# Optimization experiments

Hardware: AMD Instinct MI355X
Metric: run time of the kernel (lower is better)

Reference implementation:

```python
import jax, jax.numpy as jnp
import numpy as np
import math

NQ = 12          # num_qubits
DEPTH = 4        # circuit_depth
DIM = 2 ** NQ    # state_dim = 4096
B = 4096         # batch

# CNOT ladder: (i,i+1) plus wrap-around (n-1,0) when n>2 (as in _init_circuit_parameters)
CNOT_PAIRS = [(i, i + 1) for i in range(NQ - 1)] + ([(NQ - 1, 0)] if NQ > 2 else [])


def _rx(theta):
    c = jnp.cos(theta / 2).astype(jnp.complex64)
    s = jnp.sin(theta / 2).astype(jnp.complex64) * (-1j)
    return jnp.stack([jnp.stack([c, s]), jnp.stack([s, c])])


def _ry(phi):
    c = jnp.cos(phi / 2).astype(jnp.complex64)
    s = jnp.sin(phi / 2).astype(jnp.complex64)
    return jnp.stack([jnp.stack([c, -s]), jnp.stack([s, c])])


def _rz(lam):
    lamc = lam.astype(jnp.complex64)
    e0 = jnp.exp(-1j * lamc / 2)
    e1 = jnp.exp(1j * lamc / 2)
    z = jnp.zeros((), jnp.complex64)
    return jnp.stack([jnp.stack([e0, z]), jnp.stack([z, e1])])


def _apply_1q(state, gate, q):
    # state: [B] + [2]*NQ, qubit q lives on axis q+1 (kron order: qubit 0 most significant)
    ax = q + 1
    s = jnp.moveaxis(state, ax, -1)
    s = jnp.einsum('ab,...b->...a', gate, s)
    return jnp.moveaxis(s, -1, ax)


def _apply_cnot(state, control, target):
    # flip target bit on the control=1 half of the state vector
    ac, at = control + 1, target + 1
    s0 = jnp.take(state, jnp.array([0]), axis=ac)
    s1 = jnp.take(state, jnp.array([1]), axis=ac)
    s1 = jnp.flip(s1, axis=at)
    return jnp.concatenate([s0, s1], axis=ac)


def setup_inputs() -> dict:
    key = jax.random.key(0)
    k1, k2, k3, k4 = jax.random.split(key, 4)
    return {
        'input_data': jax.random.normal(k1, (B, DIM), dtype=jnp.float32),
        'angles_x': jax.random.normal(k2, (DEPTH, NQ), dtype=jnp.float32) * 0.5,
        'angles_y': jax.random.normal(k3, (DEPTH, NQ), dtype=jnp.float32) * 0.5,
        'angles_z': jax.random.normal(k4, (DEPTH, NQ), dtype=jnp.float32) * 0.5,
    }


def reference(input_data, angles_x, angles_y, angles_z):
    # --- amplitude encoding (faithful to quantum_weight_memory) ---
    w = jnp.abs(input_data[:, :DIM])                      # [B, D]
    D = w.shape[1]
    s = jnp.sum(w, axis=1, keepdims=True)
    wn = jnp.where(s > 1e-8, w / jnp.sqrt(jnp.maximum(s, 1e-8)),
                   jnp.full_like(w, 1.0 / math.sqrt(D)))
    state = jnp.zeros((w.shape[0], DIM), jnp.complex64).at[:, 0].set(1.0)
    state = state.at[:, :D].set(wn.astype(jnp.complex64))
    norm = jnp.sqrt(jnp.sum(jnp.abs(state) ** 2, axis=1, keepdims=True))
    state = jnp.where(norm > 1e-8, state / jnp.maximum(norm, 1e-8), state)

    # --- parametrized circuit, applied as local state-vector updates ---
    state = state.reshape((state.shape[0],) + (2,) * NQ)
    for layer in range(DEPTH):
        for q in range(NQ):
            state = _apply_1q(state, _rx(angles_x[layer, q]), q)
            state = _apply_1q(state, _ry(angles_y[layer, q]), q)
            state = _apply_1q(state, _rz(angles_z[layer, q]), q)
        for c, t in CNOT_PAIRS:
            state = _apply_cnot(state, c, t)
    state = state.reshape(-1, DIM)

    # --- measurement ---
    probs = jnp.abs(state) ** 2
    return jnp.sqrt(probs[:, :DIM])
```

## Files before the change

kernel.cpp:

```cpp
#include <hip/hip_runtime.h>
#include <math.h>

#define DIM 4096

typedef _Float16 v8h __attribute__((ext_vector_type(8)));
typedef _Float16 v4h __attribute__((ext_vector_type(4)));
typedef float v4f __attribute__((ext_vector_type(4)));
typedef unsigned int v2u __attribute__((ext_vector_type(2)));

__device__ __forceinline__ int adr(int row, int off) {
  return ((row << 6) | off) ^ ((((row >> 1) ^ (row >> 5)) & 3) << 4)
                            ^ (((row >> 4) & 1) << 6);
}


template <int PASS, bool FOLD>
__device__ __forceinline__ void do_pass(const char* __restrict__ src, char* __restrict__ dst,
                                        const v8h* __restrict__ Af, int mat, int t) {
  const int lane = t & 63, wv = t >> 6;
  const int m = lane & 15, q = lane >> 4;
  const int qb = q & 1, pm = q >> 1;
  const v8h b_re = Af[(mat * 2 + 0) * 64 + lane];
  const v8h b_im = Af[(mat * 2 + 1) * 64 + lane];
  const int gm = (m ^ (m >> 1)) & 15;
#pragma unroll
  for (int tt = 0; tt < 4; ++tt) {
    const int t4 = wv * 4 + tt;
    v8h a;
    if constexpr (PASS == 0 && FOLD) {
      const int t4g = t4 ^ (t4 >> 1);
      const bool qs = ((qb ^ tt) & 1) != 0;
      const int off = pm * 32 + (qs ? 16 : 0);
      const int r0 = ((t4g ^ ((m & 1) << 3)) << 4) | gm;
      const uint4 E = *(const uint4*)(src + adr(r0, off));
      const uint4 O = *(const uint4*)(src + adr(r0 ^ 8, off));
      const unsigned e0 = qs ? E.z : E.x, e1 = qs ? E.w : E.y;
      const unsigned e2 = qs ? E.y : E.w, e3 = qs ? E.x : E.z;
      const unsigned o0 = qs ? O.z : O.x, o1 = qs ? O.w : O.y;
      const unsigned o2 = qs ? O.y : O.w, o3 = qs ? O.x : O.z;
      uint4 av;
      av.x = __builtin_amdgcn_perm(o0, e0, 0x07060100u);
      av.y = __builtin_amdgcn_perm(o1, e1, 0x05040302u);
      av.z = __builtin_amdgcn_perm(o2, e2, 0x07060100u);
      av.w = __builtin_amdgcn_perm(o3, e3, 0x05040302u);
      a = __builtin_bit_cast(v8h, av);
    } else if constexpr (PASS == 0) {
      a = *(const v8h*)(src + adr(t4 * 16 + m, pm * 32 + qb * 16));
    } else {
      const uint4 r = *(const uint4*)(src + adr(t4 * 16 + m, (2 * qb + pm) * 16));
      const v2u s0 = __builtin_amdgcn_permlane32_swap(r.x, r.z, false, false);
      const v2u s1 = __builtin_amdgcn_permlane32_swap(r.y, r.w, false, false);
      uint4 av;
      av.x = s0.x; av.y = s1.x; av.z = s0.y; av.w = s1.y;
      a = __builtin_bit_cast(v8h, av);
    }
    const v4f cre = __builtin_amdgcn_mfma_f32_16x16x32_f16(a, b_re, (v4f){0.f, 0.f, 0.f, 0.f}, 0, 0, 0);
    const v4f cim = __builtin_amdgcn_mfma_f32_16x16x32_f16(a, b_im, (v4f){0.f, 0.f, 0.f, 0.f}, 0, 0, 0);
    const int wrow = m * 16 + t4;
    if constexpr (PASS < 2) {
      v8h w;
#pragma unroll
      for (int r2 = 0; r2 < 4; ++r2) {
        w[r2] = (_Float16)cre[r2];
        w[4 + r2] = (_Float16)cim[r2];
      }
      *(v8h*)(dst + adr(wrow, q * 16)) = w;
    } else {
      v4h wre, wim;
#pragma unroll
      for (int r2 = 0; r2 < 4; ++r2) {
        wre[r2] = (_Float16)cre[r2];
        wim[r2] = (_Float16)cim[r2];
      }
      *(v4h*)(dst + adr(wrow, q * 8)) = wre;
      *(v4h*)(dst + adr(wrow, 32 + q * 8)) = wim;
    }
  }
}

__global__ void make_gates2(const float* __restrict__ ax, const float* __restrict__ ay,
                            const float* __restrict__ az, _Float16* __restrict__ Aw) {
  __shared__ float g4[48][4];
  const int id = threadIdx.x;
  if (id < 48) {
    float th = 0.5f * ax[id], ph = 0.5f * ay[id], lm = 0.5f * az[id];
    float c = cosf(th), s = sinf(th);
    float cy = cosf(ph), sy = sinf(ph);
    float cl = cosf(lm), sl = sinf(lm);
    float m00r = cy * c, m00i = sy * s;
    float m01r = -sy * c, m01i = -cy * s;
    g4[id][0] = cl * m00r + sl * m00i;
    g4[id][1] = cl * m00i - sl * m00r;
    g4[id][2] = cl * m01r + sl * m01i;
    g4[id][3] = cl * m01i - sl * m01r;
  }
  __syncthreads();
  const int mat = id >> 6, lane = id & 63;
  const int m = lane & 15, q = lane >> 4;
  const int layer = mat / 3, pass = mat % 3, qbase = pass * 4;
#pragma unroll
  for (int j = 0; j < 8; ++j) {
    const int k = q * 8 + j, kk = k & 15;
    float cr = 1.f, ci = 0.f;
#pragma unroll
    for (int bp = 3; bp >= 0; --bp) {
      const int qq = qbase + (3 - bp);
      const int ib = (m >> bp) & 1, kb = (kk >> bp) & 1;
      const float* gg = g4[layer * 12 + qq];
      float er, ei;
      if (ib == 0 && kb == 0) { er = gg[0]; ei = gg[1]; }
      else if (ib == 0 && kb == 1) { er = gg[2]; ei = gg[3]; }
      else if (ib == 1 && kb == 0) { er = -gg[2]; ei = gg[3]; }
      else { er = gg[0]; ei = -gg[1]; }
      const float nr = cr * er - ci * ei, ni = cr * ei + ci * er;
      cr = nr; ci = ni;
    }
    const float reval = (k < 16) ? cr : -ci;
    const float imval = (k < 16) ? ci : cr;
    Aw[((mat * 2 + 0) * 64 + lane) * 8 + j] = (_Float16)reval;
    Aw[((mat * 2 + 1) * 64 + lane) * 8 + j] = (_Float16)imval;
  }
}

__global__ __launch_bounds__(256, 4) void qsim4(const float* __restrict__ x,
                                                const v8h* __restrict__ Af,
                                                float* __restrict__ out) {
  __shared__ __align__(16) char buf[2][16384];
  const int t = threadIdx.x;
  const int b = blockIdx.x;
  const float* xb = x + (size_t)b * DIM;

  float w[16];
  float sw = 0.f, sw2 = 0.f;
#pragma unroll
  for (int j = 0; j < 16; ++j) {
    float aa = fabsf(xb[t + (j << 8)]);
    w[j] = aa; sw += aa; sw2 += aa * aa;
  }
#pragma unroll
  for (int off = 32; off; off >>= 1) {
    sw += __shfl_down(sw, off, 64);
    sw2 += __shfl_down(sw2, off, 64);
  }
  float* red = (float*)buf[1];
  if ((t & 63) == 0) { red[t >> 6] = sw; red[4 + (t >> 6)] = sw2; }
  __syncthreads();
  sw = (red[0] + red[1]) + (red[2] + red[3]);
  sw2 = (red[4] + red[5]) + (red[6] + red[7]);

  float sc = 0.f;
  const bool ok = (sw > 1e-8f);
  if (ok) {
    float wnscale = rsqrtf(fmaxf(sw, 1e-8f));
    float norm = sqrtf(sw2 / sw);
    sc = ((norm > 1e-8f) ? (wnscale / fmaxf(norm, 1e-8f)) : wnscale) * 64.0f;
  }
  {
    const int row = ((t & 15) << 4) | (t >> 4);
    v8h h0, h1, z;
#pragma unroll
    for (int j = 0; j < 8; ++j) {
      h0[j] = (_Float16)(ok ? w[j] * sc : 1.0f);
      h1[j] = (_Float16)(ok ? w[8 + j] * sc : 1.0f);
      z[j] = (_Float16)0.f;
    }
    *(v8h*)(buf[0] + adr(row, 0)) = h0;
    *(v8h*)(buf[0] + adr(row, 16)) = h1;
    *(v8h*)(buf[0] + adr(row, 32)) = z;
    *(v8h*)(buf[0] + adr(row, 48)) = z;
  }
  __syncthreads();

  char* s = buf[0];
  char* d = buf[1];
  do_pass<0, false>(s, d, Af, 0, t); __syncthreads();
  do_pass<1, false>(d, s, Af, 1, t); __syncthreads();
  do_pass<2, false>(s, d, Af, 2, t); __syncthreads();
  { char* tmp = s; s = d; d = tmp; }
#pragma unroll 1
  for (int l = 1; l < 4; ++l) {
    do_pass<0, true>(s, d, Af, l * 3 + 0, t); __syncthreads();
    do_pass<1, false>(d, s, Af, l * 3 + 1, t); __syncthreads();
    do_pass<2, false>(s, d, Af, l * 3 + 2, t); __syncthreads();
    char* tmp = s; s = d; d = tmp;
  }

  float* ob = out + (size_t)b * DIM;
  {
    const int g = t ^ (t >> 1);
    const int re_row = (g & 15) * 16 + ((g >> 4) & 15);
    const int ro = re_row ^ 8;
    const int offA = (t & 1) ? 24 : 0;
    const int offB = (t & 1) ? 16 : 8;
    const v4h E0 = *(const v4h*)(s + adr(re_row, offA));
    const v4h E1 = *(const v4h*)(s + adr(re_row, offB));
    const v4h E2 = *(const v4h*)(s + adr(re_row, offA ^ 24));
    const v4h E3 = *(const v4h*)(s + adr(re_row, offB ^ 24));
    const v4h O0 = *(const v4h*)(s + adr(ro, offA));
    const v4h O1 = *(const v4h*)(s + adr(ro, offB));
    const v4h O2 = *(const v4h*)(s + adr(ro, offA ^ 24));
    const v4h O3 = *(const v4h*)(s + adr(ro, offB ^ 24));
    const v4h IE0 = *(const v4h*)(s + adr(re_row, 32 + offA));
    const v4h IE1 = *(const v4h*)(s + adr(re_row, 32 + offB));
    const v4h IE2 = *(const v4h*)(s + adr(re_row, 32 + (offA ^ 24)));
    const v4h IE3 = *(const v4h*)(s + adr(re_row, 32 + (offB ^ 24)));
    const v4h IO0 = *(const v4h*)(s + adr(ro, 32 + offA));
    const v4h IO1 = *(const v4h*)(s + adr(ro, 32 + offB));
    const v4h IO2 = *(const v4h*)(s + adr(ro, 32 + (offA ^ 24)));
    const v4h IO3 = *(const v4h*)(s + adr(ro, 32 + (offB ^ 24)));
#define MAG(J, VR, VI, IDX)                                           \
  {                                                                   \
    const float re_ = (float)VR[IDX], im_ = (float)VI[IDX];           \
    ob[((J) << 8) | t] = sqrtf(re_ * re_ + im_ * im_) * 0.015625f;    \
  }
    MAG(0, E0, IE0, 0)  MAG(2, E0, IE0, 3)  MAG(4, E1, IE1, 2)  MAG(6, E1, IE1, 1)
    MAG(8, E2, IE2, 0)  MAG(10, E2, IE2, 3) MAG(12, E3, IE3, 2) MAG(14, E3, IE3, 1)
    MAG(1, O0, IO0, 1)  MAG(3, O0, IO0, 2)  MAG(5, O1, IO1, 3)  MAG(7, O1, IO1, 0)
    MAG(9, O2, IO2, 1)  MAG(11, O2, IO2, 2) MAG(13, O3, IO3, 3) MAG(15, O3, IO3, 0)
#undef MAG
  }
}

extern "C" void kernel_launch(void* const* d_in, const int* in_sizes, int n_in,
                              void* d_out, int out_size, void* d_ws, size_t ws_size,
                              hipStream_t stream) {
  const float* x = (const float*)d_in[0];
  const float* ax = (const float*)d_in[1];
  const float* ay = (const float*)d_in[2];
  const float* az = (const float*)d_in[3];
  _Float16* Aw = (_Float16*)d_ws;
  make_gates2<<<1, 768, 0, stream>>>(ax, ay, az, Aw);
  qsim4<<<4096, 256, 0, stream>>>(x, (const v8h*)Aw, (float*)d_out);
}
```

Baseline: 159.0 us.

## Interleave re/im in shared layout, drop perm shuffles, use packed f16 converts

Pass-2 outputs are now stored with real and imaginary parts interleaved, except in the final layer. The matching pass-0 fold load becomes plain 32-bit selects instead of byte-perm merges, and the gate-matrix builder reorders its K index to fit the new layout. All float-to-half stores use packed round-toward-zero converts, and the final magnitude uses the raw hardware sqrt. The goal is to cut VALU work per pass in a kernel that is bound on LDS and ALU. The trade-off is slightly different rounding (RTZ instead of RNE), and correctness depends on the new layout and the new gate matrices agreeing.

Measured after the change: 154.9 us. -2.6%, faster.

```diff
diff --git a/kernel.cpp b/kernel.cpp
--- a/kernel.cpp
+++ b/kernel.cpp
@@ -4,9 +4,12 @@
 #define DIM 4096
 
 typedef _Float16 v8h __attribute__((ext_vector_type(8)));
-typedef _Float16 v4h __attribute__((ext_vector_type(4)));
 typedef float v4f __attribute__((ext_vector_type(4)));
 typedef unsigned int v2u __attribute__((ext_vector_type(2)));
+
+__device__ __forceinline__ unsigned pkrtz(float a, float b) {
+  return __builtin_bit_cast(unsigned, __builtin_amdgcn_cvt_pkrtz(a, b));
+}
 
 __device__ __forceinline__ int adr(int row, int off) {
   return ((row << 6) | off) ^ ((((row >> 1) ^ (row >> 5)) & 3) << 4)
@@ -14,7 +17,7 @@
 }
 
 
-template <int PASS, bool FOLD>
+template <int PASS, bool FOLD, bool LAST>
 __device__ __forceinline__ void do_pass(const char* __restrict__ src, char* __restrict__ dst,
                                         const v8h* __restrict__ Af, int mat, int t) {
   const int lane = t & 63, wv = t >> 6;
@@ -23,29 +26,25 @@
   const v8h b_re = Af[(mat * 2 + 0) * 64 + lane];
   const v8h b_im = Af[(mat * 2 + 1) * 64 + lane];
   const int gm = (m ^ (m >> 1)) & 15;
+  const bool qh = (q & 1) != 0;
 #pragma unroll
   for (int tt = 0; tt < 4; ++tt) {
     const int t4 = wv * 4 + tt;
     v8h a;
     if constexpr (PASS == 0 && FOLD) {
       const int t4g = t4 ^ (t4 >> 1);
-      const bool qs = ((qb ^ tt) & 1) != 0;
-      const int off = pm * 32 + (qs ? 16 : 0);
+      const int gq2 = ((q ^ (q >> 1)) & 3) ^ ((tt & 1) ? 3 : 0);
       const int r0 = ((t4g ^ ((m & 1) << 3)) << 4) | gm;
-      const uint4 E = *(const uint4*)(src + adr(r0, off));
-      const uint4 O = *(const uint4*)(src + adr(r0 ^ 8, off));
-      const unsigned e0 = qs ? E.z : E.x, e1 = qs ? E.w : E.y;
-      const unsigned e2 = qs ? E.y : E.w, e3 = qs ? E.x : E.z;
-      const unsigned o0 = qs ? O.z : O.x, o1 = qs ? O.w : O.y;
-      const unsigned o2 = qs ? O.y : O.w, o3 = qs ? O.x : O.z;
+      const uint4 E = *(const uint4*)(src + adr(r0, gq2 * 16));
+      const uint4 O = *(const uint4*)(src + adr(r0 ^ 8, gq2 * 16));
       uint4 av;
-      av.x = __builtin_amdgcn_perm(o0, e0, 0x07060100u);
-      av.y = __builtin_amdgcn_perm(o1, e1, 0x05040302u);
-      av.z = __builtin_amdgcn_perm(o2, e2, 0x07060100u);
-      av.w = __builtin_amdgcn_perm(o3, e3, 0x05040302u);
+      av.x = qh ? E.z : E.x;
+      av.y = qh ? O.w : O.y;
+      av.z = qh ? E.y : E.w;
+      av.w = qh ? O.x : O.z;
       a = __builtin_bit_cast(v8h, av);
     } else if constexpr (PASS == 0) {
-      a = *(const v8h*)(src + adr(t4 * 16 + m, pm * 32 + qb * 16));
+      a = *(const v8h*)(src + adr(t4 * 16 + m, q * 16));
     } else {
       const uint4 r = *(const uint4*)(src + adr(t4 * 16 + m, (2 * qb + pm) * 16));
       const v2u s0 = __builtin_amdgcn_permlane32_swap(r.x, r.z, false, false);
@@ -58,22 +57,27 @@
     const v4f cim = __builtin_amdgcn_mfma_f32_16x16x32_f16(a, b_im, (v4f){0.f, 0.f, 0.f, 0.f}, 0, 0, 0);
     const int wrow = m * 16 + t4;
     if constexpr (PASS < 2) {
-      v8h w;
-#pragma unroll
-      for (int r2 = 0; r2 < 4; ++r2) {
-        w[r2] = (_Float16)cre[r2];
-        w[4 + r2] = (_Float16)cim[r2];
-      }
-      *(v8h*)(dst + adr(wrow, q * 16)) = w;
+      uint4 w;
+      w.x = pkrtz(cre[0], cre[1]);
+      w.y = pkrtz(cre[2], cre[3]);
+      w.z = pkrtz(cim[0], cim[1]);
+      w.w = pkrtz(cim[2], cim[3]);
+      *(uint4*)(dst + adr(wrow, q * 16)) = w;
+    } else if constexpr (!LAST) {
+      uint4 w;
+      w.x = pkrtz(cre[0], cim[0]);
+      w.y = pkrtz(cre[1], cim[1]);
+      w.z = pkrtz(cre[2], cim[2]);
+      w.w = pkrtz(cre[3], cim[3]);
+      *(uint4*)(dst + adr(wrow, q * 16)) = w;
     } else {
-      v4h wre, wim;
-#pragma unroll
-      for (int r2 = 0; r2 < 4; ++r2) {
-        wre[r2] = (_Float16)cre[r2];
-        wim[r2] = (_Float16)cim[r2];
-      }
-      *(v4h*)(dst + adr(wrow, q * 8)) = wre;
-      *(v4h*)(dst + adr(wrow, 32 + q * 8)) = wim;
+      uint2 wr, wi;
+      wr.x = pkrtz(cre[0], cre[1]);
+      wr.y = pkrtz(cre[2], cre[3]);
+      wi.x = pkrtz(cim[0], cim[1]);
+      wi.y = pkrtz(cim[2], cim[3]);
+      *(uint2*)(dst + adr(wrow, q * 8)) = wr;
+      *(uint2*)(dst + adr(wrow, 32 + q * 8)) = wi;
     }
   }
 }
@@ -100,12 +104,14 @@
   const int layer = mat / 3, pass = mat % 3, qbase = pass * 4;
 #pragma unroll
   for (int j = 0; j < 8; ++j) {
-    const int k = q * 8 + j, kk = k & 15;
+    int p, ty;
+    if (pass == 0) { p = q * 4 + (j >> 1); ty = j & 1; }
+    else { p = (q * 8 + j) & 15; ty = (q >= 2) ? 1 : 0; }
     float cr = 1.f, ci = 0.f;
 #pragma unroll
     for (int bp = 3; bp >= 0; --bp) {
       const int qq = qbase + (3 - bp);
-      const int ib = (m >> bp) & 1, kb = (kk >> bp) & 1;
+      const int ib = (m >> bp) & 1, kb = (p >> bp) & 1;
       const float* gg = g4[layer * 12 + qq];
       float er, ei;
       if (ib == 0 && kb == 0) { er = gg[0]; ei = gg[1]; }
@@ -115,14 +121,14 @@
       const float nr = cr * er - ci * ei, ni = cr * ei + ci * er;
       cr = nr; ci = ni;
     }
-    const float reval = (k < 16) ? cr : -ci;
-    const float imval = (k < 16) ? ci : cr;
+    const float reval = ty ? -ci : cr;
+    const float imval = ty ? cr : ci;
     Aw[((mat * 2 + 0) * 64 + lane) * 8 + j] = (_Float16)reval;
     Aw[((mat * 2 + 1) * 64 + lane) * 8 + j] = (_Float16)imval;
   }
 }
 
-__global__ __launch_bounds__(256, 4) void qsim4(const float* __restrict__ x,
+__global__ __launch_bounds__(256, 4) void qsim5(const float* __restrict__ x,
                                                 const v8h* __restrict__ Af,
                                                 float* __restrict__ out) {
   __shared__ __align__(16) char buf[2][16384];
@@ -130,12 +136,12 @@
   const int b = blockIdx.x;
   const float* xb = x + (size_t)b * DIM;
 
-  float w[16];
+  float wa[16];
   float sw = 0.f, sw2 = 0.f;
 #pragma unroll
   for (int j = 0; j < 16; ++j) {
     float aa = fabsf(xb[t + (j << 8)]);
-    w[j] = aa; sw += aa; sw2 += aa * aa;
+    wa[j] = aa; sw += aa; sw2 += aa * aa;
   }
 #pragma unroll
   for (int off = 32; off; off >>= 1) {
@@ -155,36 +161,40 @@
     float norm = sqrtf(sw2 / sw);
     sc = ((norm > 1e-8f) ? (wnscale / fmaxf(norm, 1e-8f)) : wnscale) * 64.0f;
   }
+  const float off0 = ok ? 0.f : 1.f;
   {
     const int row = ((t & 15) << 4) | (t >> 4);
-    v8h h0, h1, z;
-#pragma unroll
-    for (int j = 0; j < 8; ++j) {
-      h0[j] = (_Float16)(ok ? w[j] * sc : 1.0f);
-      h1[j] = (_Float16)(ok ? w[8 + j] * sc : 1.0f);
-      z[j] = (_Float16)0.f;
-    }
-    *(v8h*)(buf[0] + adr(row, 0)) = h0;
-    *(v8h*)(buf[0] + adr(row, 16)) = h1;
-    *(v8h*)(buf[0] + adr(row, 32)) = z;
-    *(v8h*)(buf[0] + adr(row, 48)) = z;
+#pragma unroll
+    for (int Q = 0; Q < 4; ++Q) {
+      uint4 w;
+      w.x = pkrtz(fmaf(wa[Q * 4 + 0], sc, off0), 0.f);
+      w.y = pkrtz(fmaf(wa[Q * 4 + 1], sc, off0), 0.f);
+      w.z = pkrtz(fmaf(wa[Q * 4 + 2], sc, off0), 0.f);
+      w.w = pkrtz(fmaf(wa[Q * 4 + 3], sc, off0), 0.f);
+      *(uint4*)(buf[0] + adr(row, Q * 16)) = w;
+    }
   }
   __syncthreads();
 
   char* s = buf[0];
   char* d = buf[1];
-  do_pass<0, false>(s, d, Af, 0, t); __syncthreads();
-  do_pass<1, false>(d, s, Af, 1, t); __syncthreads();
-  do_pass<2, false>(s, d, Af, 2, t); __syncthreads();
+  do_pass<0, false, false>(s, d, Af, 0, t); __syncthreads();
+  do_pass<1, false, false>(d, s, Af, 1, t); __syncthreads();
+  do_pass<2, false, false>(s, d, Af, 2, t); __syncthreads();
   { char* tmp = s; s = d; d = tmp; }
 #pragma unroll 1
-  for (int l = 1; l < 4; ++l) {
-    do_pass<0, true>(s, d, Af, l * 3 + 0, t); __syncthreads();
-    do_pass<1, false>(d, s, Af, l * 3 + 1, t); __syncthreads();
-    do_pass<2, false>(s, d, Af, l * 3 + 2, t); __syncthreads();
+  for (int l = 1; l < 3; ++l) {
+    do_pass<0, true, false>(s, d, Af, l * 3 + 0, t); __syncthreads();
+    do_pass<1, false, false>(d, s, Af, l * 3 + 1, t); __syncthreads();
+    do_pass<2, false, false>(s, d, Af, l * 3 + 2, t); __syncthreads();
     char* tmp = s; s = d; d = tmp;
   }
-
+  do_pass<0, true, false>(s, d, Af, 9, t); __syncthreads();
+  do_pass<1, false, false>(d, s, Af, 10, t); __syncthreads();
+  do_pass<2, false, true>(s, d, Af, 11, t); __syncthreads();
+  { char* tmp = s; s = d; d = tmp; }
+
+  typedef _Float16 v4h __attribute__((ext_vector_type(4)));
   float* ob = out + (size_t)b * DIM;
   {
     const int g = t ^ (t >> 1);
@@ -208,10 +218,10 @@
     const v4h IO1 = *(const v4h*)(s + adr(ro, 32 + offB));
     const v4h IO2 = *(const v4h*)(s + adr(ro, 32 + (offA ^ 24)));
     const v4h IO3 = *(const v4h*)(s + adr(ro, 32 + (offB ^ 24)));
-#define MAG(J, VR, VI, IDX)                                           \
-  {                                                                   \
-    const float re_ = (float)VR[IDX], im_ = (float)VI[IDX];           \
-    ob[((J) << 8) | t] = sqrtf(re_ * re_ + im_ * im_) * 0.015625f;    \
+#define MAG(J, VR, VI, IDX)                                                       \
+  {                                                                               \
+    const float re_ = (float)VR[IDX], im_ = (float)VI[IDX];                       \
+    ob[((J) << 8) | t] = __builtin_amdgcn_sqrtf(re_ * re_ + im_ * im_) * 0.015625f; \
   }
     MAG(0, E0, IE0, 0)  MAG(2, E0, IE0, 3)  MAG(4, E1, IE1, 2)  MAG(6, E1, IE1, 1)
     MAG(8, E2, IE2, 0)  MAG(10, E2, IE2, 3) MAG(12, E3, IE3, 2) MAG(14, E3, IE3, 1)
@@ -230,5 +240,5 @@
   const float* az = (const float*)d_in[3];
   _Float16* Aw = (_Float16*)d_ws;
   make_gates2<<<1, 768, 0, stream>>>(ax, ay, az, Aw);
-  qsim4<<<4096, 256, 0, stream>>>(x, (const v8h*)Aw, (float*)d_out);
-}
+  qsim5<<<4096, 256, 0, stream>>>(x, (const v8h*)Aw, (float*)d_out);
+}
```
